# Optimization experiments

Measured on AMD Instinct MI355X. Metric: run time of the kernel, lower is better.

## Reference

```python
import jax, jax.numpy as jnp
import numpy as np

DIM = 128
H = 8
HD = DIM // H
NL = 6
DFF = 2048
EPS = 1e-5
S2S_STEPS = 6


def _ln(x, g, b):
    m = jnp.mean(x, -1, keepdims=True)
    v = jnp.mean(jnp.square(x - m), -1, keepdims=True)
    return (x - m) / jnp.sqrt(v + EPS) * g + b


def _lstm_step(x, h, c, wih, whh, bih, bhh):
    # torch LSTM gate order: i, f, g, o
    gates = x @ wih.T + bih + h @ whh.T + bhh
    i, f, g, o = jnp.split(gates, 4, axis=-1)
    c = jax.nn.sigmoid(f) * c + jax.nn.sigmoid(i) * jnp.tanh(g)
    h = jax.nn.sigmoid(o) * jnp.tanh(c)
    return h, c


def setup_inputs() -> dict:
    key = jax.random.key(0)
    ks = iter(jax.random.split(key, 16))
    n = lambda shape: jax.random.normal(next(ks), shape, jnp.float32) * 0.02
    inp = {
        "data": jax.random.normal(next(ks), (64, 256, 3), jnp.float32),
        "lin0_w": n((DIM, 3)), "lin0_b": jnp.zeros((DIM,), jnp.float32),
        "attn_in_w": n((NL, 3 * DIM, DIM)), "attn_in_b": jnp.zeros((NL, 3 * DIM), jnp.float32),
        "attn_out_w": n((NL, DIM, DIM)), "attn_out_b": jnp.zeros((NL, DIM), jnp.float32),
        "ln1_g": jnp.ones((NL, DIM), jnp.float32), "ln1_b": jnp.zeros((NL, DIM), jnp.float32),
        "ff_w1": n((NL, DFF, DIM)), "ff_b1": jnp.zeros((NL, DFF), jnp.float32),
        "ff_w2": n((NL, DIM, DFF)), "ff_b2": jnp.zeros((NL, DIM), jnp.float32),
        "ln2_g": jnp.ones((NL, DIM), jnp.float32), "ln2_b": jnp.zeros((NL, DIM), jnp.float32),
        "s2s_wih": n((4 * DIM, 2 * DIM)), "s2s_whh": n((4 * DIM, DIM)),
        "s2s_bih": jnp.zeros((4 * DIM,), jnp.float32), "s2s_bhh": jnp.zeros((4 * DIM,), jnp.float32),
        "mem_wih": n((4 * DIM, 2 * DIM)), "mem_whh": n((4 * DIM, DIM)),
        "mem_bih": jnp.zeros((4 * DIM,), jnp.float32), "mem_bhh": jnp.zeros((4 * DIM,), jnp.float32),
        "lin1_w": n((DIM, DIM)), "lin1_b": jnp.zeros((DIM,), jnp.float32),
        "lin3_w": n((1, DIM)), "lin3_b": jnp.zeros((1,), jnp.float32),
    }
    return inp


def reference(data, lin0_w, lin0_b, attn_in_w, attn_in_b, attn_out_w, attn_out_b,
              ln1_g, ln1_b, ff_w1, ff_b1, ff_w2, ff_b2, ln2_g, ln2_b,
              s2s_wih, s2s_whh, s2s_bih, s2s_bhh,
              mem_wih, mem_whh, mem_bih, mem_bhh,
              lin1_w, lin1_b, lin3_w, lin3_b):
    x = jax.nn.relu(data @ lin0_w.T + lin0_b)  # [S=64, B=256, D]
    S, B, _ = x.shape
    # torch TransformerEncoder with batch_first=False: attention over axis 0,
    # axis 1 is the transformer batch. Post-norm layers (norm_first=False), relu FFN.
    for l in range(NL):
        qkv = x @ attn_in_w[l].T + attn_in_b[l]
        q, k, v = jnp.split(qkv, 3, axis=-1)
        q = q.reshape(S, B, H, HD)
        k = k.reshape(S, B, H, HD)
        v = v.reshape(S, B, H, HD)
        scores = jnp.einsum('sbhd,tbhd->bhst', q, k) / np.float32(np.sqrt(HD))
        attn = jax.nn.softmax(scores, axis=-1)
        ao = jnp.einsum('bhst,tbhd->sbhd', attn, v).reshape(S, B, DIM)
        x = _ln(x + ao @ attn_out_w[l].T + attn_out_b[l], ln1_g[l], ln1_b[l])
        ff = jax.nn.relu(x @ ff_w1[l].T + ff_b1[l]) @ ff_w2[l].T + ff_b2[l]
        x = _ln(x + ff, ln2_g[l], ln2_b[l])
    # Set2Set pooling: bidxs assign segment = axis-0 index for each block of
    # num_atoms consecutive rows of flatten(out,0,1), i.e. pool over axis 1.
    q_star = jnp.zeros((S, 2 * DIM), x.dtype)
    h = jnp.zeros((S, DIM), x.dtype)
    c = jnp.zeros((S, DIM), x.dtype)
    for _ in range(S2S_STEPS):
        h, c = _lstm_step(q_star, h, c, s2s_wih, s2s_whh, s2s_bih, s2s_bhh)
        e = jnp.einsum('bnd,bd->bn', x, h)          # [S, num_atoms]
        a = jax.nn.softmax(e, axis=-1)              # segment softmax (uniform segs)
        r = jnp.einsum('bn,bnd->bd', a, x)          # segment weighted sum
        q_star = jnp.concatenate([h, r], axis=-1)   # [S, 2D]
    # memory LSTM: seq_len 1, zero initial state (states=None branch)
    hx = jnp.zeros((S, DIM), x.dtype)
    cx = jnp.zeros((S, DIM), x.dtype)
    hx, cx = _lstm_step(q_star, hx, cx, mem_wih, mem_whh, mem_bih, mem_bhh)
    o = jax.nn.relu(hx @ lin1_w.T + lin1_b)
    v_out = (o @ lin3_w.T + lin3_b)[None]  # [1, S, 1]
    return v_out, hx[None], cx[None]
```

## Files before the change

kernel.cpp:

```cpp
#include <hip/hip_runtime.h>
#include <math.h>


typedef _Float16 __attribute__((ext_vector_type(8))) f16x8;
typedef __attribute__((ext_vector_type(4))) float f32x4;
typedef _Float16 __attribute__((ext_vector_type(2))) h16x2;

__device__ __forceinline__ unsigned short f2h(float f) {
  union { _Float16 h; unsigned short s; } x; x.h = (_Float16)f; return x.s;
}
__device__ __forceinline__ float h2f(unsigned short u) {
  union { unsigned short s; _Float16 h; } x; x.s = u; return (float)x.h;
}
__device__ __forceinline__ unsigned packh(float a, float b) {
  return (unsigned)f2h(a) | ((unsigned)f2h(b) << 16);
}
__device__ __forceinline__ float hlo(unsigned u) {
  union { unsigned short s; _Float16 h; } x; x.s = (unsigned short)(u & 0xffff);
  return (float)x.h;
}
__device__ __forceinline__ float hhi(unsigned u) {
  union { unsigned short s; _Float16 h; } x; x.s = (unsigned short)(u >> 16);
  return (float)x.h;
}
__device__ __forceinline__ float fdot2u(unsigned a, unsigned b, float c) {
#if __has_builtin(__builtin_amdgcn_fdot2)
  union U { unsigned u; h16x2 h; };
  U x, y; x.u = a; y.u = b;
  return __builtin_amdgcn_fdot2(x.h, y.h, c, false);
#else
  return c + hlo(a) * hlo(b) + hhi(a) * hhi(b);
#endif
}
__device__ __forceinline__ float sigf(float x) { return 1.f / (1.f + expf(-x)); }

__device__ __forceinline__ void gl2lds16(const void* g, void* l) {
  __builtin_amdgcn_global_load_lds(
      (const __attribute__((address_space(1))) unsigned int*)g,
      (__attribute__((address_space(3))) unsigned int*)l, 16, 0, 0);
}

__global__ __launch_bounds__(256) void convw_kernel(
    const float* __restrict__ aiw, const float* __restrict__ aow,
    const float* __restrict__ w1, const float* __restrict__ w2,
    const float* __restrict__ wih, const float* __restrict__ whh,
    const float* __restrict__ mwih,
    unsigned short* __restrict__ o0, unsigned short* __restrict__ o1,
    unsigned short* __restrict__ o2, unsigned short* __restrict__ o3,
    unsigned short* __restrict__ o4, unsigned short* __restrict__ o5,
    unsigned short* __restrict__ o6) {
  int i = blockIdx.x * 256 + threadIdx.x;
  if (i < 294912) {
    int l = i / 49152, o = i % 49152;
    int j = o & 7, fr = (o >> 3) & 15, fq = (o >> 7) & 3, ks = (o >> 9) & 3,
        rb = o >> 11;
    o0[i] = f2h(aiw[l * 49152 + (rb * 16 + fr) * 128 + ks * 32 + fq * 8 + j]);
  } else if (i < 393216) {
    int ii = i - 294912;
    int l = ii / 16384, o = ii % 16384;
    int j = o & 7, fr = (o >> 3) & 15, fq = (o >> 7) & 3, ks = (o >> 9) & 3,
        rb = o >> 11;
    o1[ii] = f2h(aow[l * 16384 + (rb * 16 + fr) * 128 + ks * 32 + fq * 8 + j]);
  } else if (i < 1966080) {
    int ii = i - 393216;
    int l = ii >> 18, o = ii & 262143;
    int j = o & 7, fr = (o >> 3) & 15, fq = (o >> 7) & 3, ks = (o >> 9) & 3,
        rb = o >> 11;
    o2[ii] = f2h(w1[l * 262144 + (rb * 16 + fr) * 128 + ks * 32 + fq * 8 + j]);
  } else if (i < 3538944) {
    int ii = i - 1966080;
    int l = ii >> 18, o = ii & 262143;
    int j = o & 7, fr = (o >> 3) & 15, fq = (o >> 7) & 3, ks = (o >> 9) & 63,
        rb = o >> 15;
    o3[ii] = f2h(w2[l * 262144 + (rb * 16 + fr) * 2048 + ks * 32 + fq * 8 + j]);
  } else if (i < 3670016) {
    int j = i - 3538944; o4[j] = f2h(wih[j]);
  } else if (i < 3735552) {
    int j = i - 3670016; o5[j] = f2h(whh[j]);
  } else {
    int j = i - 3735552; o6[j] = f2h(mwih[j]);
  }
}

__global__ __launch_bounds__(256) void lin0_kernel(
    const float* __restrict__ data, const float* __restrict__ w,
    const float* __restrict__ b, float* __restrict__ x,
    unsigned short* __restrict__ xb) {
  int i = blockIdx.x * 256 + threadIdx.x;
  int n = i >> 7, d = i & 127;
  float v = b[d] + data[n * 3 + 0] * w[d * 3 + 0]
                 + data[n * 3 + 1] * w[d * 3 + 1]
                 + data[n * 3 + 2] * w[d * 3 + 2];
  v = fmaxf(v, 0.0f);
  x[i] = v;
  xb[i] = f2h(v);
}

__global__ __launch_bounds__(256, 2) void layer_kernel(
    const unsigned short* __restrict__ xbg,
    const unsigned short* __restrict__ wqkv, const float* __restrict__ bqkv,
    const unsigned short* __restrict__ wout, const float* __restrict__ bout,
    const float* __restrict__ ln1g, const float* __restrict__ ln1b,
    const unsigned short* __restrict__ w1, const float* __restrict__ b1,
    const unsigned short* __restrict__ w2, const float* __restrict__ b2,
    const float* __restrict__ ln2g, const float* __restrict__ ln2b,
    float* __restrict__ xio, unsigned short* __restrict__ xbo) {
  __shared__ __align__(16) unsigned short Xs[64 * 128];
  __shared__ __align__(16) unsigned short QKP[16384];
  __shared__ __align__(16) unsigned short VT[128 * 64];
  __shared__ __align__(16) uint4 zchunk;
  __shared__ float psum[4][32], psq[4][32];
  __shared__ float2 stats[32];

  unsigned short* Qs = QKP;
  unsigned short* Ks2 = QKP + 8192;

  int tid = threadIdx.x, w = tid >> 6, lane = tid & 63;
  int b = blockIdx.x >> 1, half = blockIdx.x & 1;
  int r4 = lane >> 4, cs = lane & 15;
  int fr = lane & 15, fq = lane >> 4;

  if (tid == 0) zchunk = make_uint4(0u, 0u, 0u, 0u);

#pragma unroll
  for (int i = 0; i < 4; i++) {
    int issue = w * 4 + i;
    int row = issue * 4 + r4;
    int g = cs ^ (row & 7);
    gl2lds16(xbg + (size_t)(row * 256 + b) * 128 + g * 8,
             (char*)Xs + issue * 1024);
  }
  __syncthreads();

  f16x8 xfragA[4][4];
#pragma unroll
  for (int ks = 0; ks < 4; ks++)
#pragma unroll
    for (int mi = 0; mi < 4; mi++) {
      int row = mi * 16 + fr;
      int kq = (ks * 4 + fq) ^ (row & 7);
      xfragA[ks][mi] = *(const f16x8*)(Xs + row * 128 + kq * 8);
    }

  {
    f32x4 acc[4][4];
#pragma unroll
    for (int i = 0; i < 4; i++)
#pragma unroll
      for (int j = 0; j < 4; j++) acc[i][j] = (f32x4){0.f, 0.f, 0.f, 0.f};
#pragma unroll
    for (int ks = 0; ks < 4; ks++) {
      f16x8 bf[4];
#pragma unroll
      for (int ni = 0; ni < 4; ni++)
        bf[ni] = *(const f16x8*)(wqkv + (w * 4 + ni) * 2048 + ks * 512 +
                                 fq * 128 + fr * 8);
#pragma unroll
      for (int mi = 0; mi < 4; mi++)
#pragma unroll
        for (int ni = 0; ni < 4; ni++)
          acc[mi][ni] = __builtin_amdgcn_mfma_f32_16x16x32_f16(
              xfragA[ks][mi], bf[ni], acc[mi][ni], 0, 0, 0);
    }
#pragma unroll
    for (int ni = 0; ni < 4; ni++) {
      int c = (w * 4 + ni) * 16 + fr;
      float bv = bqkv[c];
      unsigned short* dst = (c < 128) ? Qs : Ks2;
      int cc = c & 127;
#pragma unroll
      for (int mi = 0; mi < 4; mi++)
#pragma unroll
        for (int r = 0; r < 4; r++) {
          int row = mi * 16 + fq * 4 + r;
          dst[row * 128 + (((cc >> 3) ^ (row & 7)) << 3) + (cc & 7)] =
              f2h(acc[mi][ni][r] + bv);
        }
    }
  }
  __syncthreads();

  {
    f32x4 acc[2][4];
#pragma unroll
    for (int i = 0; i < 2; i++)
#pragma unroll
      for (int j = 0; j < 4; j++) acc[i][j] = (f32x4){0.f, 0.f, 0.f, 0.f};
#pragma unroll
    for (int ks = 0; ks < 4; ks++) {
      f16x8 bf[2];
#pragma unroll
      for (int fi = 0; fi < 2; fi++)
        bf[fi] = *(const f16x8*)(wqkv + (16 + w * 2 + fi) * 2048 + ks * 512 +
                                 fq * 128 + fr * 8);
#pragma unroll
      for (int fi = 0; fi < 2; fi++)
#pragma unroll
        for (int mi = 0; mi < 4; mi++)
          acc[fi][mi] = __builtin_amdgcn_mfma_f32_16x16x32_f16(
              xfragA[ks][mi], bf[fi], acc[fi][mi], 0, 0, 0);
    }
#pragma unroll
    for (int fi = 0; fi < 2; fi++) {
      int f = (w * 2 + fi) * 16 + fr;
      float bv = bqkv[256 + f];
#pragma unroll
      for (int mi = 0; mi < 4; mi++)
#pragma unroll
        for (int r = 0; r < 4; r++) {
          int srow = mi * 16 + fq * 4 + r;
          VT[f * 64 + (((srow >> 3) ^ (f & 7)) << 3) + (srow & 7)] =
              f2h(acc[fi][mi][r] + bv);
        }
    }
  }
  __syncthreads();

  {
    f16x8 afH[2][2], bfH[2][4];
#pragma unroll
    for (int hi = 0; hi < 2; hi++) {
      int h = w * 2 + hi;
#pragma unroll
      for (int mi2 = 0; mi2 < 2; mi2++) {
        int rowg = half * 32 + mi2 * 16 + fr;
        const unsigned short* pa =
            (fq < 2) ? (Qs + rowg * 128 + (((h * 2 + fq) ^ (rowg & 7)) << 3))
                     : (const unsigned short*)&zchunk;
        afH[hi][mi2] = *(const f16x8*)pa;
      }
#pragma unroll
      for (int ti = 0; ti < 4; ti++) {
        int trow = ti * 16 + fr;
        const unsigned short* pb =
            (fq < 2) ? (Ks2 + trow * 128 + (((h * 2 + fq) ^ (trow & 7)) << 3))
                     : (const unsigned short*)&zchunk;
        bfH[hi][ti] = *(const f16x8*)pb;
      }
    }
    __syncthreads();

#pragma unroll
    for (int hi = 0; hi < 2; hi++) {
      int h = w * 2 + hi;
      unsigned short* Pb = QKP + (w * 2 + hi) * 2048;
      f32x4 sc[2][4];
#pragma unroll
      for (int i = 0; i < 2; i++)
#pragma unroll
        for (int j = 0; j < 4; j++) sc[i][j] = (f32x4){0.f, 0.f, 0.f, 0.f};
#pragma unroll
      for (int mi2 = 0; mi2 < 2; mi2++)
#pragma unroll
        for (int ti = 0; ti < 4; ti++)
          sc[mi2][ti] = __builtin_amdgcn_mfma_f32_16x16x32_f16(
              afH[hi][mi2], bfH[hi][ti], sc[mi2][ti], 0, 0, 0);
#pragma unroll
      for (int mi2 = 0; mi2 < 2; mi2++) {
#pragma unroll
        for (int r = 0; r < 4; r++) {
          float m = -1e30f;
#pragma unroll
          for (int ti = 0; ti < 4; ti++) m = fmaxf(m, sc[mi2][ti][r]);
          m = fmaxf(m, __shfl_xor(m, 1, 64));
          m = fmaxf(m, __shfl_xor(m, 2, 64));
          m = fmaxf(m, __shfl_xor(m, 4, 64));
          m = fmaxf(m, __shfl_xor(m, 8, 64));
          m *= 0.25f;
          float ss = 0.f;
#pragma unroll
          for (int ti = 0; ti < 4; ti++) {
            float p = expf(sc[mi2][ti][r] * 0.25f - m);
            sc[mi2][ti][r] = p;
            ss += p;
          }
          ss += __shfl_xor(ss, 1, 64);
          ss += __shfl_xor(ss, 2, 64);
          ss += __shfl_xor(ss, 4, 64);
          ss += __shfl_xor(ss, 8, 64);
          float inv = 1.f / ss;
          int prow = mi2 * 16 + fq * 4 + r;
#pragma unroll
          for (int ti = 0; ti < 4; ti++) {
            int t = ti * 16 + fr;
            Pb[prow * 64 + (((t >> 3) ^ (prow & 7)) << 3) + (t & 7)] =
                f2h(sc[mi2][ti][r] * inv);
          }
        }
      }
      f32x4 po[2];
#pragma unroll
      for (int i = 0; i < 2; i++) po[i] = (f32x4){0.f, 0.f, 0.f, 0.f};
#pragma unroll
      for (int ks2 = 0; ks2 < 2; ks2++) {
        f16x8 af[2], bf;
#pragma unroll
        for (int si2 = 0; si2 < 2; si2++) {
          int prow = si2 * 16 + fr;
          int kq = (ks2 * 4 + fq) ^ (prow & 7);
          af[si2] = *(const f16x8*)(Pb + prow * 64 + kq * 8);
        }
        {
          int vrow = h * 16 + fr;
          int kq = (ks2 * 4 + fq) ^ (vrow & 7);
          bf = *(const f16x8*)(VT + vrow * 64 + kq * 8);
        }
#pragma unroll
        for (int si2 = 0; si2 < 2; si2++)
          po[si2] = __builtin_amdgcn_mfma_f32_16x16x32_f16(af[si2], bf,
                                                           po[si2], 0, 0, 0);
      }
#pragma unroll
      for (int si2 = 0; si2 < 2; si2++)
#pragma unroll
        for (int r = 0; r < 4; r++) {
          int arow = si2 * 16 + fq * 4 + r;
          int c = h * 16 + fr;
          Xs[arow * 128 + (((c >> 3) ^ (arow & 7)) << 3) + (c & 7)] =
              f2h(po[si2][r]);
        }
    }
  }
  __syncthreads();

  float vv4[2][2][4];
  {
    f32x4 acc[2][2];
#pragma unroll
    for (int i = 0; i < 2; i++)
#pragma unroll
      for (int j = 0; j < 2; j++) acc[i][j] = (f32x4){0.f, 0.f, 0.f, 0.f};
#pragma unroll
    for (int ks = 0; ks < 4; ks++) {
      f16x8 af[2], bwo[2];
#pragma unroll
      for (int si2 = 0; si2 < 2; si2++) {
        int rowl = si2 * 16 + fr;
        int kq = (ks * 4 + fq) ^ (rowl & 7);
        af[si2] = *(const f16x8*)(Xs + rowl * 128 + kq * 8);
      }
#pragma unroll
      for (int ni = 0; ni < 2; ni++)
        bwo[ni] = *(const f16x8*)(wout + (w * 2 + ni) * 2048 + ks * 512 +
                                  fq * 128 + fr * 8);
#pragma unroll
      for (int si2 = 0; si2 < 2; si2++)
#pragma unroll
        for (int ni = 0; ni < 2; ni++)
          acc[si2][ni] = __builtin_amdgcn_mfma_f32_16x16x32_f16(
              af[si2], bwo[ni], acc[si2][ni], 0, 0, 0);
    }
    float sums[2][4], sqs[2][4];
#pragma unroll
    for (int si2 = 0; si2 < 2; si2++)
#pragma unroll
      for (int r = 0; r < 4; r++) { sums[si2][r] = 0.f; sqs[si2][r] = 0.f; }
#pragma unroll
    for (int ni = 0; ni < 2; ni++) {
      int c = (w * 2 + ni) * 16 + fr;
      float bv = bout[c];
#pragma unroll
      for (int si2 = 0; si2 < 2; si2++)
#pragma unroll
        for (int r = 0; r < 4; r++) {
          int rowl = si2 * 16 + fq * 4 + r;
          int rowg = half * 32 + rowl;
          float v = acc[si2][ni][r] + bv + xio[(size_t)(rowg * 256 + b) * 128 + c];
          vv4[ni][si2][r] = v;
          sums[si2][r] += v;
          sqs[si2][r] += v * v;
        }
    }
#pragma unroll
    for (int d = 1; d < 16; d <<= 1) {
#pragma unroll
      for (int si2 = 0; si2 < 2; si2++)
#pragma unroll
        for (int r = 0; r < 4; r++) {
          sums[si2][r] += __shfl_xor(sums[si2][r], d, 64);
          sqs[si2][r] += __shfl_xor(sqs[si2][r], d, 64);
        }
    }
    if (fr == 0) {
#pragma unroll
      for (int si2 = 0; si2 < 2; si2++)
#pragma unroll
        for (int r = 0; r < 4; r++) {
          int rowl = si2 * 16 + fq * 4 + r;
          psum[w][rowl] = sums[si2][r];
          psq[w][rowl] = sqs[si2][r];
        }
    }
    __syncthreads();
    if (tid < 32) {
      float S = 0.f, Q = 0.f;
#pragma unroll
      for (int ww = 0; ww < 4; ww++) { S += psum[ww][tid]; Q += psq[ww][tid]; }
      float m = S * (1.f / 128.f);
      float var = Q * (1.f / 128.f) - m * m;
      stats[tid] = make_float2(m, rsqrtf(var + 1e-5f));
    }
    __syncthreads();
#pragma unroll
    for (int ni = 0; ni < 2; ni++) {
      int c = (w * 2 + ni) * 16 + fr;
      float gl = ln1g[c], bl = ln1b[c];
#pragma unroll
      for (int si2 = 0; si2 < 2; si2++)
#pragma unroll
        for (int r = 0; r < 4; r++) {
          int rowl = si2 * 16 + fq * 4 + r;
          float2 st2 = stats[rowl];
          float y = (vv4[ni][si2][r] - st2.x) * st2.y * gl + bl;
          Xs[rowl * 128 + (((c >> 3) ^ (rowl & 7)) << 3) + (c & 7)] = f2h(y);
        }
    }
  }
  __syncthreads();

  f16x8 xfragF[4][2];
#pragma unroll
  for (int ks = 0; ks < 4; ks++)
#pragma unroll
    for (int mi2 = 0; mi2 < 2; mi2++) {
      int rowl = mi2 * 16 + fr;
      int kq = (ks * 4 + fq) ^ (rowl & 7);
      xfragF[ks][mi2] = *(const f16x8*)(Xs + rowl * 128 + kq * 8);
    }

  f32x4 acc2[2][2];
#pragma unroll
  for (int i = 0; i < 2; i++)
#pragma unroll
    for (int j = 0; j < 2; j++) acc2[i][j] = (f32x4){0.f, 0.f, 0.f, 0.f};

  for (int c = 0; c < 16; c++) {
    unsigned short* Hcur = QKP + (c & 1) * 4096;
    f32x4 acc1[2][2];
#pragma unroll
    for (int i = 0; i < 2; i++)
#pragma unroll
      for (int j = 0; j < 2; j++) acc1[i][j] = (f32x4){0.f, 0.f, 0.f, 0.f};
#pragma unroll
    for (int ks = 0; ks < 4; ks++) {
      f16x8 b1f[2];
#pragma unroll
      for (int ni = 0; ni < 2; ni++)
        b1f[ni] = *(const f16x8*)(w1 + (size_t)(c * 8 + w * 2 + ni) * 2048 +
                                  ks * 512 + fq * 128 + fr * 8);
#pragma unroll
      for (int mi2 = 0; mi2 < 2; mi2++)
#pragma unroll
        for (int ni = 0; ni < 2; ni++)
          acc1[mi2][ni] = __builtin_amdgcn_mfma_f32_16x16x32_f16(
              xfragF[ks][mi2], b1f[ni], acc1[mi2][ni], 0, 0, 0);
    }
#pragma unroll
    for (int ni = 0; ni < 2; ni++) {
      int col = (w * 2 + ni) * 16 + fr;
      float bv = b1[c * 128 + col];
#pragma unroll
      for (int mi2 = 0; mi2 < 2; mi2++)
#pragma unroll
        for (int r = 0; r < 4; r++) {
          int rowl = mi2 * 16 + fq * 4 + r;
          Hcur[rowl * 128 + (((col >> 3) ^ (rowl & 7)) << 3) + (col & 7)] =
              f2h(fmaxf(acc1[mi2][ni][r] + bv, 0.f));
        }
    }
    __syncthreads();
#pragma unroll
    for (int ks = 0; ks < 4; ks++) {
      f16x8 af[2], b2f[2];
#pragma unroll
      for (int si2 = 0; si2 < 2; si2++) {
        int rowl = si2 * 16 + fr;
        int kq = (ks * 4 + fq) ^ (rowl & 7);
        af[si2] = *(const f16x8*)(Hcur + rowl * 128 + kq * 8);
      }
#pragma unroll
      for (int ni = 0; ni < 2; ni++)
        b2f[ni] = *(const f16x8*)(w2 + (size_t)(w * 2 + ni) * 32768 +
                                  (c * 4 + ks) * 512 + fq * 128 + fr * 8);
#pragma unroll
      for (int si2 = 0; si2 < 2; si2++)
#pragma unroll
        for (int ni = 0; ni < 2; ni++)
          acc2[si2][ni] = __builtin_amdgcn_mfma_f32_16x16x32_f16(
              af[si2], b2f[ni], acc2[si2][ni], 0, 0, 0);
    }
  }

  {
    float vvo[2][2][4];
    float sums[2][4], sqs[2][4];
#pragma unroll
    for (int si2 = 0; si2 < 2; si2++)
#pragma unroll
      for (int r = 0; r < 4; r++) { sums[si2][r] = 0.f; sqs[si2][r] = 0.f; }
#pragma unroll
    for (int ni = 0; ni < 2; ni++) {
      int c = (w * 2 + ni) * 16 + fr;
      float bv = b2[c];
#pragma unroll
      for (int si2 = 0; si2 < 2; si2++)
#pragma unroll
        for (int r = 0; r < 4; r++) {
          int rowl = si2 * 16 + fq * 4 + r;
          float resid =
              h2f(Xs[rowl * 128 + (((c >> 3) ^ (rowl & 7)) << 3) + (c & 7)]);
          float v = acc2[si2][ni][r] + bv + resid;
          vvo[ni][si2][r] = v;
          sums[si2][r] += v;
          sqs[si2][r] += v * v;
        }
    }
#pragma unroll
    for (int d = 1; d < 16; d <<= 1) {
#pragma unroll
      for (int si2 = 0; si2 < 2; si2++)
#pragma unroll
        for (int r = 0; r < 4; r++) {
          sums[si2][r] += __shfl_xor(sums[si2][r], d, 64);
          sqs[si2][r] += __shfl_xor(sqs[si2][r], d, 64);
        }
    }
    if (fr == 0) {
#pragma unroll
      for (int si2 = 0; si2 < 2; si2++)
#pragma unroll
        for (int r = 0; r < 4; r++) {
          int rowl = si2 * 16 + fq * 4 + r;
          psum[w][rowl] = sums[si2][r];
          psq[w][rowl] = sqs[si2][r];
        }
    }
    __syncthreads();
    if (tid < 32) {
      float S = 0.f, Q = 0.f;
#pragma unroll
      for (int ww = 0; ww < 4; ww++) { S += psum[ww][tid]; Q += psq[ww][tid]; }
      float m = S * (1.f / 128.f);
      float var = Q * (1.f / 128.f) - m * m;
      stats[tid] = make_float2(m, rsqrtf(var + 1e-5f));
    }
    __syncthreads();
#pragma unroll
    for (int ni = 0; ni < 2; ni++) {
      int c = (w * 2 + ni) * 16 + fr;
      float gl = ln2g[c], bl = ln2b[c];
#pragma unroll
      for (int si2 = 0; si2 < 2; si2++)
#pragma unroll
        for (int r = 0; r < 4; r++) {
          int rowl = si2 * 16 + fq * 4 + r;
          float2 st = stats[rowl];
          float y = (vvo[ni][si2][r] - st.x) * st.y * gl + bl;
          size_t o = (size_t)((half * 32 + rowl) * 256 + b) * 128 + c;
          xio[o] = y;
          xbo[o] = f2h(y);
        }
    }
  }
}

__global__ __launch_bounds__(512, 1) void s2s_kernel(
    const unsigned short* __restrict__ xb,
    const unsigned short* __restrict__ wihh,
    const unsigned short* __restrict__ whhh,
    const float* __restrict__ bih, const float* __restrict__ bhh,
    const unsigned short* __restrict__ mwihh,
    const float* __restrict__ mbih, const float* __restrict__ mbhh,
    const float* __restrict__ l1w, const float* __restrict__ l1b,
    const float* __restrict__ l3w, const float* __restrict__ l3b,
    float* __restrict__ out) {
  __shared__ __align__(16) unsigned xl[256 * 65];
  __shared__ __align__(16) unsigned qu[128];
  __shared__ __align__(16) float cst[128];
  __shared__ __align__(16) float gates[512];
  __shared__ __align__(16) float red[256];
  __shared__ __align__(16) float aw[256];
  int s = blockIdx.x, t = threadIdx.x, lane = t & 63, w = t >> 6;

  uint4 wreg[32], ureg[16];
  {
    const uint4* wp = (const uint4*)(wihh + (size_t)t * 256);
#pragma unroll
    for (int i = 0; i < 32; i++) wreg[i] = wp[i];
    const uint4* up = (const uint4*)(whhh + (size_t)t * 128);
#pragma unroll
    for (int i = 0; i < 16; i++) ureg[i] = up[i];
  }

  const uint4* xs4 = (const uint4*)(xb + (size_t)s * 32768);
#pragma unroll
  for (int it = 0; it < 8; it++) {
    int f = it * 512 + t;
    uint4 v = xs4[f];
    int n = f >> 4, jc = (f & 15) * 4;
    unsigned* dst = xl + n * 65 + jc;
    dst[0] = v.x; dst[1] = v.y; dst[2] = v.z; dst[3] = v.w;
  }
  if (t < 128) cst[t] = 0.f;
  __syncthreads();

  const uint4* q4 = (const uint4*)qu;
  float bsum = bih[t] + bhh[t];

  for (int step = 0; step < 6; step++) {
    if (step > 0) {
      float a0 = 0.f, a1 = 0.f, a2 = 0.f, a3 = 0.f;
#pragma unroll
      for (int i = 0; i < 16; i++) {
        uint4 qv = q4[i];
        a0 = fdot2u(wreg[i].x, qv.x, a0);
        a1 = fdot2u(wreg[i].y, qv.y, a1);
        a2 = fdot2u(wreg[i].z, qv.z, a2);
        a3 = fdot2u(wreg[i].w, qv.w, a3);
        a0 = fdot2u(ureg[i].x, qv.x, a0);
        a1 = fdot2u(ureg[i].y, qv.y, a1);
        a2 = fdot2u(ureg[i].z, qv.z, a2);
        a3 = fdot2u(ureg[i].w, qv.w, a3);
      }
#pragma unroll
      for (int i = 16; i < 32; i++) {
        uint4 qv = q4[i];
        a0 = fdot2u(wreg[i].x, qv.x, a0);
        a1 = fdot2u(wreg[i].y, qv.y, a1);
        a2 = fdot2u(wreg[i].z, qv.z, a2);
        a3 = fdot2u(wreg[i].w, qv.w, a3);
      }
      gates[t] = bsum + ((a0 + a1) + (a2 + a3));
    } else {
      gates[t] = bsum;
    }
    __syncthreads();
    if (t < 128) {
      float ig = sigf(gates[t]), fg = sigf(gates[128 + t]);
      float gg = tanhf(gates[256 + t]), og = sigf(gates[384 + t]);
      float cn = fg * cst[t] + ig * gg;
      cst[t] = cn;
      float hn = og * tanhf(cn);
      float hp = __shfl_xor(hn, 1, 64);
      if ((t & 1) == 0) qu[t >> 1] = packh(hn, hp);
    }
    __syncthreads();
    if (step > 0) {
      int n = t >> 1, p = t & 1;
      const unsigned* xr = xl + n * 65 + p * 32;
      float e0 = 0.f, e1 = 0.f;
#pragma unroll 8
      for (int i = 0; i < 32; i += 2) {
        e0 = fdot2u(xr[i], qu[p * 32 + i], e0);
        e1 = fdot2u(xr[i + 1], qu[p * 32 + i + 1], e1);
      }
      float e = e0 + e1;
      e += __shfl_xor(e, 1, 64);
      if (p == 0) red[n] = e;
      __syncthreads();
      float v0 = red[lane], v1 = red[64 + lane];
      float v2 = red[128 + lane], v3 = red[192 + lane];
      float m = fmaxf(fmaxf(v0, v1), fmaxf(v2, v3));
#pragma unroll
      for (int d = 1; d < 64; d <<= 1) m = fmaxf(m, __shfl_xor(m, d, 64));
      float p0 = expf(v0 - m), p1 = expf(v1 - m);
      float p2 = expf(v2 - m), p3 = expf(v3 - m);
      float ss = p0 + p1 + p2 + p3;
#pragma unroll
      for (int d = 1; d < 64; d <<= 1) ss += __shfl_xor(ss, d, 64);
      float Sinv = 1.f / ss;
      if (w == 0) {
        aw[lane] = p0 * Sinv; aw[64 + lane] = p1 * Sinv;
        aw[128 + lane] = p2 * Sinv; aw[192 + lane] = p3 * Sinv;
      }
    } else {
      if (t < 256) aw[t] = 1.f / 256.f;
    }
    __syncthreads();
    {
      int d = t & 127, grp = t >> 7;
      const unsigned* xc = xl + grp * 64 * 65 + (d >> 1);
      int hi = d & 1;
      const float* ap = aw + grp * 64;
      float r = 0.f;
#pragma unroll 8
      for (int n2 = 0; n2 < 64; n2++) {
        unsigned u = xc[n2 * 65];
        r += ap[n2] * (hi ? hhi(u) : hlo(u));
      }
      gates[t] = r;
    }
    __syncthreads();
    if (t < 128) {
      float rd = gates[t] + gates[128 + t] + gates[256 + t] + gates[384 + t];
      float rp = __shfl_xor(rd, 1, 64);
      if ((t & 1) == 0) qu[64 + (t >> 1)] = packh(rd, rp);
    }
    __syncthreads();
  }
  {
    float a0 = 0.f, a1 = 0.f, a2 = 0.f, a3 = 0.f;
    const uint4* mp = (const uint4*)(mwihh + (size_t)t * 256);
#pragma unroll 8
    for (int i = 0; i < 32; i++) {
      uint4 wv = mp[i], qv = q4[i];
      a0 = fdot2u(wv.x, qv.x, a0);
      a1 = fdot2u(wv.y, qv.y, a1);
      a2 = fdot2u(wv.z, qv.z, a2);
      a3 = fdot2u(wv.w, qv.w, a3);
    }
    gates[t] = mbih[t] + mbhh[t] + ((a0 + a1) + (a2 + a3));
  }
  __syncthreads();
  if (t < 128) {
    float ig = sigf(gates[t]);
    float gg = tanhf(gates[256 + t]);
    float og = sigf(gates[384 + t]);
    float cx = ig * gg;
    float hx = og * tanhf(cx);
    cst[t] = hx;
    out[64 + s * 128 + t] = hx;
    out[64 + 8192 + s * 128 + t] = cx;
  }
  __syncthreads();
  if (t < 128) {
    float acc = l1b[t];
    const float4* w4 = (const float4*)(l1w + (size_t)t * 128);
    const float4* h4 = (const float4*)cst;
#pragma unroll 8
    for (int k = 0; k < 32; k++) {
      float4 a = w4[k], b = h4[k];
      acc += a.x * b.x + a.y * b.y + a.z * b.z + a.w * b.w;
    }
    red[t] = fmaxf(acc, 0.f) * l3w[t];
  } else if (t < 256) {
    red[t] = 0.f;
  }
  __syncthreads();
  for (int off = 128; off; off >>= 1) {
    if (t < off) red[t] += red[t + off];
    __syncthreads();
  }
  if (t == 0) out[s] = red[0] + l3b[0];
}

extern "C" void kernel_launch(void* const* d_in, const int* in_sizes, int n_in,
                              void* d_out, int out_size, void* d_ws,
                              size_t ws_size, hipStream_t stream) {
  const float* data       = (const float*)d_in[0];
  const float* lin0_w     = (const float*)d_in[1];
  const float* lin0_b     = (const float*)d_in[2];
  const float* attn_in_w  = (const float*)d_in[3];
  const float* attn_in_b  = (const float*)d_in[4];
  const float* attn_out_w = (const float*)d_in[5];
  const float* attn_out_b = (const float*)d_in[6];
  const float* ln1_g      = (const float*)d_in[7];
  const float* ln1_b      = (const float*)d_in[8];
  const float* ff_w1      = (const float*)d_in[9];
  const float* ff_b1      = (const float*)d_in[10];
  const float* ff_w2      = (const float*)d_in[11];
  const float* ff_b2      = (const float*)d_in[12];
  const float* ln2_g      = (const float*)d_in[13];
  const float* ln2_b      = (const float*)d_in[14];
  const float* s2s_wih    = (const float*)d_in[15];
  const float* s2s_whh    = (const float*)d_in[16];
  const float* s2s_bih    = (const float*)d_in[17];
  const float* s2s_bhh    = (const float*)d_in[18];
  const float* mem_wih    = (const float*)d_in[19];
  const float* mem_bih    = (const float*)d_in[21];
  const float* mem_bhh    = (const float*)d_in[22];
  const float* lin1_w     = (const float*)d_in[23];
  const float* lin1_b     = (const float*)d_in[24];
  const float* lin3_w     = (const float*)d_in[25];
  const float* lin3_b     = (const float*)d_in[26];
  float* out = (float*)d_out;

  char* p = (char*)d_ws;
  float* x = (float*)p;                      p += (size_t)16384 * 128 * 4;
  unsigned short* xb = (unsigned short*)p;   p += (size_t)16384 * 128 * 2;
  unsigned short* wqkv = (unsigned short*)p; p += (size_t)294912 * 2;
  unsigned short* wout = (unsigned short*)p; p += (size_t)98304 * 2;
  unsigned short* w1h = (unsigned short*)p;  p += (size_t)1572864 * 2;
  unsigned short* w2h = (unsigned short*)p;  p += (size_t)1572864 * 2;
  unsigned short* wihh = (unsigned short*)p; p += (size_t)131072 * 2;
  unsigned short* whhh = (unsigned short*)p; p += (size_t)65536 * 2;
  unsigned short* mwihh = (unsigned short*)p; p += (size_t)131072 * 2;

  convw_kernel<<<15104, 256, 0, stream>>>(
      attn_in_w, attn_out_w, ff_w1, ff_w2, s2s_wih, s2s_whh, mem_wih,
      wqkv, wout, w1h, w2h, wihh, whhh, mwihh);
  lin0_kernel<<<8192, 256, 0, stream>>>(data, lin0_w, lin0_b, x, xb);

  for (int l = 0; l < 6; l++) {
    layer_kernel<<<512, 256, 0, stream>>>(
        xb, wqkv + (size_t)l * 49152, attn_in_b + l * 384,
        wout + (size_t)l * 16384, attn_out_b + l * 128,
        ln1_g + l * 128, ln1_b + l * 128,
        w1h + (size_t)l * 262144, ff_b1 + l * 2048,
        w2h + (size_t)l * 262144, ff_b2 + l * 128,
        ln2_g + l * 128, ln2_b + l * 128, x, xb);
  }

  s2s_kernel<<<64, 512, 0, stream>>>(
      xb, wihh, whhh, s2s_bih, s2s_bhh,
      mwihh, mem_bih, mem_bhh, lin1_w, lin1_b, lin3_w, lin3_b, out);
}
```

Baseline: 461.5 us.

## Split QKV projection into separate kernel to remove redundant compute per half-block

Before, each pair of blocks (two halves of a batch column) both computed the full 64-row QKV projection, duplicating that work. The projection now runs in its own kernel, one block per batch column, and writes a pre-swizzled Q/K/V^T image to a global workspace. The layer kernel loads only its half of Q plus all of K and V^T directly into LDS. That shrinks shared memory enough to raise launch bounds to three blocks per CU. The cost is an extra kernel launch per layer and an extra global round trip of about 12 MB of QKV data.

```diff
diff --git a/kernel.cpp b/kernel.cpp
--- a/kernel.cpp
+++ b/kernel.cpp
@@ -96,126 +96,138 @@
   xb[i] = f2h(v);
 }
 
-__global__ __launch_bounds__(256, 2) void layer_kernel(
+__global__ __launch_bounds__(512) void qkv_kernel(
     const unsigned short* __restrict__ xbg,
     const unsigned short* __restrict__ wqkv, const float* __restrict__ bqkv,
+    unsigned short* __restrict__ qkvg) {
+  __shared__ __align__(16) unsigned short Xs[8192];
+  __shared__ __align__(16) unsigned short img[24576];
+
+  int tid = threadIdx.x, w = tid >> 6, lane = tid & 63;
+  int b = blockIdx.x;
+  int r4 = lane >> 4, cs = lane & 15;
+  int fr = lane & 15, fq = lane >> 4;
+
+#pragma unroll
+  for (int i = 0; i < 2; i++) {
+    int issue = w * 2 + i;
+    int row = issue * 4 + r4;
+    int g = cs ^ (row & 7);
+    gl2lds16(xbg + (size_t)(row * 256 + b) * 128 + g * 8,
+             (char*)Xs + issue * 1024);
+  }
+  __syncthreads();
+
+  f32x4 acc[4][3];
+#pragma unroll
+  for (int i = 0; i < 4; i++)
+#pragma unroll
+    for (int j = 0; j < 3; j++) acc[i][j] = (f32x4){0.f, 0.f, 0.f, 0.f};
+#pragma unroll
+  for (int ks = 0; ks < 4; ks++) {
+    f16x8 bf[3];
+#pragma unroll
+    for (int ni = 0; ni < 3; ni++)
+      bf[ni] = *(const f16x8*)(wqkv + (size_t)(w * 3 + ni) * 2048 + ks * 512 +
+                               fq * 128 + fr * 8);
+    f16x8 af[4];
+#pragma unroll
+    for (int mi = 0; mi < 4; mi++) {
+      int row = mi * 16 + fr;
+      int kq = (ks * 4 + fq) ^ (row & 7);
+      af[mi] = *(const f16x8*)(Xs + row * 128 + kq * 8);
+    }
+#pragma unroll
+    for (int mi = 0; mi < 4; mi++)
+#pragma unroll
+      for (int ni = 0; ni < 3; ni++)
+        acc[mi][ni] = __builtin_amdgcn_mfma_f32_16x16x32_f16(
+            af[mi], bf[ni], acc[mi][ni], 0, 0, 0);
+  }
+#pragma unroll
+  for (int ni = 0; ni < 3; ni++) {
+    int c = (w * 3 + ni) * 16 + fr;
+    float bv = bqkv[c];
+    if (c < 128) {
+#pragma unroll
+      for (int mi = 0; mi < 4; mi++)
+#pragma unroll
+        for (int r = 0; r < 4; r++) {
+          int row = mi * 16 + fq * 4 + r;
+          int prow = row & 31;
+          img[(row >> 5) * 4096 + prow * 128 +
+              (((c >> 3) ^ (prow & 7)) << 3) + (c & 7)] =
+              f2h(acc[mi][ni][r] + bv);
+        }
+    } else if (c < 256) {
+      int cc = c - 128;
+#pragma unroll
+      for (int mi = 0; mi < 4; mi++)
+#pragma unroll
+        for (int r = 0; r < 4; r++) {
+          int row = mi * 16 + fq * 4 + r;
+          img[8192 + row * 128 + (((cc >> 3) ^ (row & 7)) << 3) + (cc & 7)] =
+              f2h(acc[mi][ni][r] + bv);
+        }
+    } else {
+      int f = c - 256;
+#pragma unroll
+      for (int mi = 0; mi < 4; mi++)
+#pragma unroll
+        for (int r = 0; r < 4; r++) {
+          int srow = mi * 16 + fq * 4 + r;
+          img[16384 + f * 64 + (((srow >> 3) ^ (f & 7)) << 3) + (srow & 7)] =
+              f2h(acc[mi][ni][r] + bv);
+        }
+    }
+  }
+  __syncthreads();
+
+  const uint4* s4 = (const uint4*)img;
+  uint4* d4 = (uint4*)(qkvg + (size_t)b * 24576);
+#pragma unroll
+  for (int i = 0; i < 6; i++) d4[i * 512 + tid] = s4[i * 512 + tid];
+}
+
+__global__ __launch_bounds__(256, 3) void layer_kernel(
+    const unsigned short* __restrict__ qkvg,
     const unsigned short* __restrict__ wout, const float* __restrict__ bout,
     const float* __restrict__ ln1g, const float* __restrict__ ln1b,
     const unsigned short* __restrict__ w1, const float* __restrict__ b1,
     const unsigned short* __restrict__ w2, const float* __restrict__ b2,
     const float* __restrict__ ln2g, const float* __restrict__ ln2b,
     float* __restrict__ xio, unsigned short* __restrict__ xbo) {
-  __shared__ __align__(16) unsigned short Xs[64 * 128];
-  __shared__ __align__(16) unsigned short QKP[16384];
-  __shared__ __align__(16) unsigned short VT[128 * 64];
-  __shared__ __align__(16) uint4 zchunk;
+  __shared__ __align__(16) unsigned short SM[20480];
   __shared__ float psum[4][32], psq[4][32];
   __shared__ float2 stats[32];
-
-  unsigned short* Qs = QKP;
-  unsigned short* Ks2 = QKP + 8192;
+  __shared__ __align__(16) uint4 zchunk;
+
+  unsigned short* Qs = SM;
+  unsigned short* Ks = SM + 4096;
+  unsigned short* VT = SM + 12288;
+  unsigned short* AOs = SM + 12288;
+  unsigned short* Xn = SM;
 
   int tid = threadIdx.x, w = tid >> 6, lane = tid & 63;
   int b = blockIdx.x >> 1, half = blockIdx.x & 1;
-  int r4 = lane >> 4, cs = lane & 15;
   int fr = lane & 15, fq = lane >> 4;
 
   if (tid == 0) zchunk = make_uint4(0u, 0u, 0u, 0u);
 
-#pragma unroll
-  for (int i = 0; i < 4; i++) {
-    int issue = w * 4 + i;
-    int row = issue * 4 + r4;
-    int g = cs ^ (row & 7);
-    gl2lds16(xbg + (size_t)(row * 256 + b) * 128 + g * 8,
-             (char*)Xs + issue * 1024);
-  }
-  __syncthreads();
-
-  f16x8 xfragA[4][4];
-#pragma unroll
-  for (int ks = 0; ks < 4; ks++)
-#pragma unroll
-    for (int mi = 0; mi < 4; mi++) {
-      int row = mi * 16 + fr;
-      int kq = (ks * 4 + fq) ^ (row & 7);
-      xfragA[ks][mi] = *(const f16x8*)(Xs + row * 128 + kq * 8);
-    }
-
-  {
-    f32x4 acc[4][4];
-#pragma unroll
-    for (int i = 0; i < 4; i++)
-#pragma unroll
-      for (int j = 0; j < 4; j++) acc[i][j] = (f32x4){0.f, 0.f, 0.f, 0.f};
-#pragma unroll
-    for (int ks = 0; ks < 4; ks++) {
-      f16x8 bf[4];
-#pragma unroll
-      for (int ni = 0; ni < 4; ni++)
-        bf[ni] = *(const f16x8*)(wqkv + (w * 4 + ni) * 2048 + ks * 512 +
-                                 fq * 128 + fr * 8);
-#pragma unroll
-      for (int mi = 0; mi < 4; mi++)
-#pragma unroll
-        for (int ni = 0; ni < 4; ni++)
-          acc[mi][ni] = __builtin_amdgcn_mfma_f32_16x16x32_f16(
-              xfragA[ks][mi], bf[ni], acc[mi][ni], 0, 0, 0);
-    }
-#pragma unroll
-    for (int ni = 0; ni < 4; ni++) {
-      int c = (w * 4 + ni) * 16 + fr;
-      float bv = bqkv[c];
-      unsigned short* dst = (c < 128) ? Qs : Ks2;
-      int cc = c & 127;
-#pragma unroll
-      for (int mi = 0; mi < 4; mi++)
-#pragma unroll
-        for (int r = 0; r < 4; r++) {
-          int row = mi * 16 + fq * 4 + r;
-          dst[row * 128 + (((cc >> 3) ^ (row & 7)) << 3) + (cc & 7)] =
-              f2h(acc[mi][ni][r] + bv);
-        }
-    }
-  }
-  __syncthreads();
-
-  {
-    f32x4 acc[2][4];
-#pragma unroll
-    for (int i = 0; i < 2; i++)
-#pragma unroll
-      for (int j = 0; j < 4; j++) acc[i][j] = (f32x4){0.f, 0.f, 0.f, 0.f};
-#pragma unroll
-    for (int ks = 0; ks < 4; ks++) {
-      f16x8 bf[2];
-#pragma unroll
-      for (int fi = 0; fi < 2; fi++)
-        bf[fi] = *(const f16x8*)(wqkv + (16 + w * 2 + fi) * 2048 + ks * 512 +
-                                 fq * 128 + fr * 8);
-#pragma unroll
-      for (int fi = 0; fi < 2; fi++)
-#pragma unroll
-        for (int mi = 0; mi < 4; mi++)
-          acc[fi][mi] = __builtin_amdgcn_mfma_f32_16x16x32_f16(
-              xfragA[ks][mi], bf[fi], acc[fi][mi], 0, 0, 0);
-    }
-#pragma unroll
-    for (int fi = 0; fi < 2; fi++) {
-      int f = (w * 2 + fi) * 16 + fr;
-      float bv = bqkv[256 + f];
-#pragma unroll
-      for (int mi = 0; mi < 4; mi++)
-#pragma unroll
-        for (int r = 0; r < 4; r++) {
-          int srow = mi * 16 + fq * 4 + r;
-          VT[f * 64 + (((srow >> 3) ^ (f & 7)) << 3) + (srow & 7)] =
-              f2h(acc[fi][mi][r] + bv);
-        }
-    }
-  }
-  __syncthreads();
-
+  const unsigned short* src = qkvg + (size_t)b * 24576;
+#pragma unroll
+  for (int i = 0; i < 10; i++) {
+    int l = w * 10 + i;
+    int soff = (l < 8 ? half * 4096 : 4096) + l * 512;
+    gl2lds16(src + soff + lane * 8, (char*)SM + l * 1024);
+  }
+  __syncthreads();
+
+  f32x4 po[2][2];
+#pragma unroll
+  for (int i = 0; i < 2; i++)
+#pragma unroll
+    for (int j = 0; j < 2; j++) po[i][j] = (f32x4){0.f, 0.f, 0.f, 0.f};
   {
     f16x8 afH[2][2], bfH[2][4];
 #pragma unroll
@@ -223,9 +235,9 @@
       int h = w * 2 + hi;
 #pragma unroll
       for (int mi2 = 0; mi2 < 2; mi2++) {
-        int rowg = half * 32 + mi2 * 16 + fr;
+        int qrow = mi2 * 16 + fr;
         const unsigned short* pa =
-            (fq < 2) ? (Qs + rowg * 128 + (((h * 2 + fq) ^ (rowg & 7)) << 3))
+            (fq < 2) ? (Qs + qrow * 128 + (((h * 2 + fq) ^ (qrow & 7)) << 3))
                      : (const unsigned short*)&zchunk;
         afH[hi][mi2] = *(const f16x8*)pa;
       }
@@ -233,17 +245,17 @@
       for (int ti = 0; ti < 4; ti++) {
         int trow = ti * 16 + fr;
         const unsigned short* pb =
-            (fq < 2) ? (Ks2 + trow * 128 + (((h * 2 + fq) ^ (trow & 7)) << 3))
+            (fq < 2) ? (Ks + trow * 128 + (((h * 2 + fq) ^ (trow & 7)) << 3))
                      : (const unsigned short*)&zchunk;
         bfH[hi][ti] = *(const f16x8*)pb;
       }
     }
     __syncthreads();
 
+    unsigned short* Pb = Ks + w * 2048;
 #pragma unroll
     for (int hi = 0; hi < 2; hi++) {
       int h = w * 2 + hi;
-      unsigned short* Pb = QKP + (w * 2 + hi) * 2048;
       f32x4 sc[2][4];
 #pragma unroll
       for (int i = 0; i < 2; i++)
@@ -288,9 +300,6 @@
           }
         }
       }
-      f32x4 po[2];
-#pragma unroll
-      for (int i = 0; i < 2; i++) po[i] = (f32x4){0.f, 0.f, 0.f, 0.f};
 #pragma unroll
       for (int ks2 = 0; ks2 < 2; ks2++) {
         f16x8 af[2], bf;
@@ -307,23 +316,26 @@
         }
 #pragma unroll
         for (int si2 = 0; si2 < 2; si2++)
-          po[si2] = __builtin_amdgcn_mfma_f32_16x16x32_f16(af[si2], bf,
-                                                           po[si2], 0, 0, 0);
-      }
-#pragma unroll
-      for (int si2 = 0; si2 < 2; si2++)
-#pragma unroll
-        for (int r = 0; r < 4; r++) {
-          int arow = si2 * 16 + fq * 4 + r;
-          int c = h * 16 + fr;
-          Xs[arow * 128 + (((c >> 3) ^ (arow & 7)) << 3) + (c & 7)] =
-              f2h(po[si2][r]);
-        }
-    }
-  }
-  __syncthreads();
-
-  float vv4[2][2][4];
+          po[hi][si2] = __builtin_amdgcn_mfma_f32_16x16x32_f16(
+              af[si2], bf, po[hi][si2], 0, 0, 0);
+      }
+    }
+  }
+  __syncthreads();
+#pragma unroll
+  for (int hi = 0; hi < 2; hi++) {
+    int c = (w * 2 + hi) * 16 + fr;
+#pragma unroll
+    for (int si2 = 0; si2 < 2; si2++)
+#pragma unroll
+      for (int r = 0; r < 4; r++) {
+        int arow = si2 * 16 + fq * 4 + r;
+        AOs[arow * 128 + (((c >> 3) ^ (arow & 7)) << 3) + (c & 7)] =
+            f2h(po[hi][si2][r]);
+      }
+  }
+  __syncthreads();
+
   {
     f32x4 acc[2][2];
 #pragma unroll
@@ -337,12 +349,12 @@
       for (int si2 = 0; si2 < 2; si2++) {
         int rowl = si2 * 16 + fr;
         int kq = (ks * 4 + fq) ^ (rowl & 7);
-        af[si2] = *(const f16x8*)(Xs + rowl * 128 + kq * 8);
+        af[si2] = *(const f16x8*)(AOs + rowl * 128 + kq * 8);
       }
 #pragma unroll
       for (int ni = 0; ni < 2; ni++)
-        bwo[ni] = *(const f16x8*)(wout + (w * 2 + ni) * 2048 + ks * 512 +
-                                  fq * 128 + fr * 8);
+        bwo[ni] = *(const f16x8*)(wout + (size_t)(w * 2 + ni) * 2048 +
+                                  ks * 512 + fq * 128 + fr * 8);
 #pragma unroll
       for (int si2 = 0; si2 < 2; si2++)
 #pragma unroll
@@ -350,6 +362,7 @@
           acc[si2][ni] = __builtin_amdgcn_mfma_f32_16x16x32_f16(
               af[si2], bwo[ni], acc[si2][ni], 0, 0, 0);
     }
+    float vv4[2][2][4];
     float sums[2][4], sqs[2][4];
 #pragma unroll
     for (int si2 = 0; si2 < 2; si2++)
@@ -365,7 +378,8 @@
         for (int r = 0; r < 4; r++) {
           int rowl = si2 * 16 + fq * 4 + r;
           int rowg = half * 32 + rowl;
-          float v = acc[si2][ni][r] + bv + xio[(size_t)(rowg * 256 + b) * 128 + c];
+          float v = acc[si2][ni][r] + bv +
+                    xio[(size_t)(rowg * 256 + b) * 128 + c];
           vv4[ni][si2][r] = v;
           sums[si2][r] += v;
           sqs[si2][r] += v * v;
@@ -412,7 +426,7 @@
           int rowl = si2 * 16 + fq * 4 + r;
           float2 st2 = stats[rowl];
           float y = (vv4[ni][si2][r] - st2.x) * st2.y * gl + bl;
-          Xs[rowl * 128 + (((c >> 3) ^ (rowl & 7)) << 3) + (c & 7)] = f2h(y);
+          Xn[rowl * 128 + (((c >> 3) ^ (rowl & 7)) << 3) + (c & 7)] = f2h(y);
         }
     }
   }
@@ -425,9 +439,10 @@
     for (int mi2 = 0; mi2 < 2; mi2++) {
       int rowl = mi2 * 16 + fr;
       int kq = (ks * 4 + fq) ^ (rowl & 7);
-      xfragF[ks][mi2] = *(const f16x8*)(Xs + rowl * 128 + kq * 8);
-    }
-
+      xfragF[ks][mi2] = *(const f16x8*)(Xn + rowl * 128 + kq * 8);
+    }
+
+  unsigned short* HsB = Ks;
   f32x4 acc2[2][2];
 #pragma unroll
   for (int i = 0; i < 2; i++)
@@ -435,7 +450,7 @@
     for (int j = 0; j < 2; j++) acc2[i][j] = (f32x4){0.f, 0.f, 0.f, 0.f};
 
   for (int c = 0; c < 16; c++) {
-    unsigned short* Hcur = QKP + (c & 1) * 4096;
+    unsigned short* Hcur = HsB + (c & 1) * 4096;
     f32x4 acc1[2][2];
 #pragma unroll
     for (int i = 0; i < 2; i++)
@@ -508,7 +523,7 @@
         for (int r = 0; r < 4; r++) {
           int rowl = si2 * 16 + fq * 4 + r;
           float resid =
-              h2f(Xs[rowl * 128 + (((c >> 3) ^ (rowl & 7)) << 3) + (c & 7)]);
+              h2f(Xn[rowl * 128 + (((c >> 3) ^ (rowl & 7)) << 3) + (c & 7)]);
           float v = acc2[si2][ni][r] + bv + resid;
           vvo[ni][si2][r] = v;
           sums[si2][r] += v;
@@ -785,6 +800,7 @@
   unsigned short* wihh = (unsigned short*)p; p += (size_t)131072 * 2;
   unsigned short* whhh = (unsigned short*)p; p += (size_t)65536 * 2;
   unsigned short* mwihh = (unsigned short*)p; p += (size_t)131072 * 2;
+  unsigned short* qkvg = (unsigned short*)p; p += (size_t)256 * 24576 * 2;
 
   convw_kernel<<<15104, 256, 0, stream>>>(
       attn_in_w, attn_out_w, ff_w1, ff_w2, s2s_wih, s2s_whh, mem_wih,
@@ -792,8 +808,10 @@
   lin0_kernel<<<8192, 256, 0, stream>>>(data, lin0_w, lin0_b, x, xb);
 
   for (int l = 0; l < 6; l++) {
+    qkv_kernel<<<256, 512, 0, stream>>>(
+        xb, wqkv + (size_t)l * 49152, attn_in_b + l * 384, qkvg);
     layer_kernel<<<512, 256, 0, stream>>>(
-        xb, wqkv + (size_t)l * 49152, attn_in_b + l * 384,
+        qkvg,
         wout + (size_t)l * 16384, attn_out_b + l * 128,
         ln1_g + l * 128, ln1_b + l * 128,
         w1h + (size_t)l * 262144, ff_b1 + l * 2048,
```

Result: slower. 491.7 us (+6.5%).
